# Kernel tuning notes

Hardware: AMD Instinct MI355X
Metric: run time of the kernel (lower is better)

Reference implementation:

```python
import jax, jax.numpy as jnp
import numpy as np

B, T, D, H, L, C = 64, 512, 256, 1024, 2, 128


def setup_inputs() -> dict:
    key = jax.random.key(0)
    ks = jax.random.split(key, 11)
    s = 0.05
    return {
        "x": jax.random.normal(ks[0], (B, T, D), dtype=jnp.float32),
        "W_ih0": jax.random.normal(ks[1], (4 * H, D), dtype=jnp.float32) * s,
        "W_hh0": jax.random.normal(ks[2], (4 * H, H), dtype=jnp.float32) * s,
        "b_ih0": jax.random.normal(ks[3], (4 * H,), dtype=jnp.float32) * s,
        "b_hh0": jax.random.normal(ks[4], (4 * H,), dtype=jnp.float32) * s,
        "W_ih1": jax.random.normal(ks[5], (4 * H, H), dtype=jnp.float32) * s,
        "W_hh1": jax.random.normal(ks[6], (4 * H, H), dtype=jnp.float32) * s,
        "b_ih1": jax.random.normal(ks[7], (4 * H,), dtype=jnp.float32) * s,
        "b_hh1": jax.random.normal(ks[8], (4 * H,), dtype=jnp.float32) * s,
        "W_fc": jax.random.normal(ks[9], (C, H), dtype=jnp.float32) * s,
        "b_fc": jax.random.normal(ks[10], (C,), dtype=jnp.float32) * s,
    }


def _lstm_cell(inp, h, c, Wi, Wh, bi, bh):
    # PyTorch LSTMCell: gates ordered i, f, g, o
    gates = inp @ Wi.T + bi + h @ Wh.T + bh  # [B, 4H]
    i, f, g, o = jnp.split(gates, 4, axis=-1)
    c_new = jax.nn.sigmoid(f) * c + jax.nn.sigmoid(i) * jnp.tanh(g)
    h_new = jax.nn.sigmoid(o) * jnp.tanh(c_new)
    return h_new, c_new


def reference(x, W_ih0, W_hh0, b_ih0, b_hh0, W_ih1, W_hh1, b_ih1, b_hh1, W_fc, b_fc):
    b = x.shape[0]
    h0 = jnp.zeros((b, H), x.dtype)
    init = (h0, h0, h0, h0)  # (h_l0, c_l0, h_l1, c_l1)

    def step(carry, x_t):
        h0_, c0_, h1_, c1_ = carry
        h0n, c0n = _lstm_cell(x_t, h0_, c0_, W_ih0, W_hh0, b_ih0, b_hh0)
        h1n, c1n = _lstm_cell(h0n, h1_, c1_, W_ih1, W_hh1, b_ih1, b_hh1)
        return (h0n, c0n, h1n, c1n), None

    xt = jnp.swapaxes(x, 0, 1)  # [T, B, D]
    (h0f, c0f, h1f, c1f), _ = jax.lax.scan(step, init, xt)
    return h1f @ W_fc.T + b_fc  # [B, num_classes]
```

## Files before the change

### kernel.cpp

```cpp
#include <hip/hip_runtime.h>
#include <hip/hip_bf16.h>

#define B_ 64
#define T_ 512
#define D_ 256
#define H_ 1024
#define RING 64
#define PS 260

typedef __attribute__((ext_vector_type(8))) short short8;
typedef __attribute__((ext_vector_type(4))) float floatx4;

__device__ __forceinline__ unsigned short f2bf(float f){
  unsigned u = __builtin_bit_cast(unsigned, f);
  u = (u + 0x7fffu + ((u >> 16) & 1u)) >> 16;
  return (unsigned short)u;
}

__device__ __forceinline__ short8 pack8(floatx4 a, floatx4 b){
  short8 r;
  r[0]=(short)f2bf(a[0]); r[1]=(short)f2bf(a[1]); r[2]=(short)f2bf(a[2]); r[3]=(short)f2bf(a[3]);
  r[4]=(short)f2bf(b[0]); r[5]=(short)f2bf(b[1]); r[6]=(short)f2bf(b[2]); r[7]=(short)f2bf(b[3]);
  return r;
}

__device__ __forceinline__ float sigm(float v){ return 1.f/(1.f+__expf(-v)); }
__device__ __forceinline__ float tanh_f(float v){ return 1.f - 2.f/(1.f+__expf(2.f*v)); }

__device__ __forceinline__ void gpoll(const unsigned long long* watch,
                                      unsigned& seen0, unsigned& seen1,
                                      unsigned tgt0, unsigned tgt1){
  if (__all(seen0 >= tgt0 && seen1 >= tgt1)) return;
  long g = 0;
  for (;;){
    unsigned long long v = __hip_atomic_load(watch, __ATOMIC_RELAXED, __HIP_MEMORY_SCOPE_AGENT);
    unsigned v0 = (unsigned)v, v1 = (unsigned)(v >> 32);
    seen0 = v0 > seen0 ? v0 : seen0;
    seen1 = v1 > seen1 ? v1 : seen1;
    if (__all(seen0 >= tgt0 && seen1 >= tgt1)) break;
    if (++g > (1L<<24)) break;
  }
}

__device__ __forceinline__ void lspin(unsigned* flag, unsigned tgt){
  long g = 0;
  while (__hip_atomic_load(flag, __ATOMIC_RELAXED, __HIP_MEMORY_SCOPE_WORKGROUP) < tgt){
    if (++g > (1L<<24)) break;
  }
}

template<int LAYER>
__device__ __forceinline__ void run_lstm(
    const float* __restrict__ x,
    const float* __restrict__ Wi, const float* __restrict__ Wh,
    const float* __restrict__ bi, const float* __restrict__ bh,
    unsigned* seq, unsigned short* h0h, unsigned short* h1h, float* h1f,
    int jbase, int j, int half,
    float* partial , float* c_st , float* biasv ,
    unsigned* rdy )
{
  constexpr int NK = LAYER ? 8 : 5;
  constexpr int KA = LAYER ? 1024 : 256;

  const int tid  = threadIdx.x;
  const int wave = tid >> 6;
  const int lane = tid & 63;
  const int n15  = lane & 15;
  const int kq   = (lane >> 4) * 8;

  short8 bfr[4][NK];
  #pragma unroll
  for (int nt = 0; nt < 4; nt++){
    int n   = nt*16 + n15;
    int row = (n >> 4)*H_ + jbase + (n & 15);
    #pragma unroll
    for (int ks = 0; ks < NK; ks++){
      int k = (LAYER ? (ks < 4 ? 1024 + wave*128 + ks*32 : wave*128 + (ks-4)*32)
                     : wave*160 + ks*32) + kq;
      const float* s = (k < KA) ? (Wi + (size_t)row*KA + k)
                                : (Wh + (size_t)row*H_ + (k - KA));
      bfr[nt][ks] = pack8(*(const floatx4*)s, *(const floatx4*)(s + 4));
    }
  }
  if (tid < 64){
    int col = (tid >> 4)*H_ + jbase + (tid & 15);
    biasv[tid] = bi[col] + bh[col];
  }
  c_st[tid & 511] = 0.f;
  if (tid == 0){ rdy[0] = 0u; rdy[1] = 0u; }
  __syncthreads();

  const unsigned long long* watch =
      (const unsigned long long*)seq + (size_t)(half*64 + lane);
  const bool isPoll = LAYER ? (wave == 0 || wave == 4) : (wave <= 1);

  unsigned seen0 = 0, seen1 = 0;
  unsigned long long vf = 0;

  for (int t = 0; t < T_; t++){
    { unsigned p0 = (unsigned)vf, p1 = (unsigned)(vf >> 32);
      seen0 = p0 > seen0 ? p0 : seen0;
      seen1 = p1 > seen1 ? p1 : seen1; }

    floatx4 acc[2][4];
    #pragma unroll
    for (int mt = 0; mt < 2; mt++)
      #pragma unroll
      for (int nt = 0; nt < 4; nt++)
        acc[mt][nt] = (floatx4)0.f;

    const unsigned short* h0t = h0h + ((size_t)((LAYER ? t : (t-1)) & (RING-1)) << 16);
    const unsigned short* h1t = h1h + ((size_t)((t-1) & (RING-1)) << 16);

    if constexpr (LAYER == 0){
      #pragma unroll
      for (int ks = 0; ks < NK; ks++){
        const int kb = wave*160 + ks*32;
        if (kb < D_){
          const int kk = kb + kq;
          short8 afr[2];
          #pragma unroll
          for (int mt = 0; mt < 2; mt++){
            const float* xs = x + ((size_t)(half*32 + mt*16 + n15)*T_ + t)*D_ + kk;
            afr[mt] = pack8(*(const floatx4*)xs, *(const floatx4*)(xs + 4));
          }
          #pragma unroll
          for (int mt = 0; mt < 2; mt++)
            #pragma unroll
            for (int nt = 0; nt < 4; nt++)
              acc[mt][nt] = __builtin_amdgcn_mfma_f32_16x16x32_bf16(afr[mt], bfr[nt][ks], acc[mt][nt], 0, 0, 0);
        }
      }
      __builtin_amdgcn_sched_barrier(0);
      if (wave == 0){
        gpoll(watch, seen0, seen1, 0u, (t >= RING) ? (unsigned)(t - RING + 1) : 0u);
      } else if (wave == 1){
        gpoll(watch, seen0, seen1, (unsigned)t, 0u);
        if (lane == 0) __hip_atomic_store(&rdy[0], (unsigned)(t + 1),
                                          __ATOMIC_RELAXED, __HIP_MEMORY_SCOPE_WORKGROUP);
      } else {
        lspin(&rdy[0], (unsigned)(t + 1));
      }
      __builtin_amdgcn_sched_barrier(0);
      if (t > 0){
        #pragma unroll
        for (int ks = 0; ks < NK; ks++){
          const int kb = wave*160 + ks*32;
          if (kb >= D_){
            const int hk = kb - D_ + kq;
            const unsigned short* p = h0t + ((hk >> 4) << 10) + (hk & 15);
            short8 afr[2];
            #pragma unroll
            for (int mt = 0; mt < 2; mt++)
              afr[mt] = *(const short8*)(p + ((half*32 + mt*16 + n15) << 4));
            #pragma unroll
            for (int mt = 0; mt < 2; mt++)
              #pragma unroll
              for (int nt = 0; nt < 4; nt++)
                acc[mt][nt] = __builtin_amdgcn_mfma_f32_16x16x32_bf16(afr[mt], bfr[nt][ks], acc[mt][nt], 0, 0, 0);
          }
        }
      }
    } else {
      if (wave == 4){
        gpoll(watch, seen0, seen1, 0u, (unsigned)t);
        if (lane == 0) __hip_atomic_store(&rdy[1], (unsigned)(t + 1),
                                          __ATOMIC_RELAXED, __HIP_MEMORY_SCOPE_WORKGROUP);
      } else {
        lspin(&rdy[1], (unsigned)(t + 1));
      }
      __builtin_amdgcn_sched_barrier(0);
      if (t > 0){
        #pragma unroll
        for (int ks = 0; ks < 4; ks++){
          const int hk = wave*128 + ks*32 + kq;
          const unsigned short* p = h1t + ((hk >> 4) << 10) + (hk & 15);
          short8 afr[2];
          #pragma unroll
          for (int mt = 0; mt < 2; mt++)
            afr[mt] = *(const short8*)(p + ((half*32 + mt*16 + n15) << 4));
          #pragma unroll
          for (int mt = 0; mt < 2; mt++)
            #pragma unroll
            for (int nt = 0; nt < 4; nt++)
              acc[mt][nt] = __builtin_amdgcn_mfma_f32_16x16x32_bf16(afr[mt], bfr[nt][ks], acc[mt][nt], 0, 0, 0);
        }
      }
      __builtin_amdgcn_sched_barrier(0);
      if (wave == 0){
        gpoll(watch, seen0, seen1, (unsigned)(t + 1), 0u);
        if (lane == 0) __hip_atomic_store(&rdy[0], (unsigned)(t + 1),
                                          __ATOMIC_RELAXED, __HIP_MEMORY_SCOPE_WORKGROUP);
      } else {
        lspin(&rdy[0], (unsigned)(t + 1));
      }
      __builtin_amdgcn_sched_barrier(0);
      #pragma unroll
      for (int ks = 4; ks < 8; ks++){
        const int hk = wave*128 + (ks-4)*32 + kq;
        const unsigned short* p = h0t + ((hk >> 4) << 10) + (hk & 15);
        short8 afr[2];
        #pragma unroll
        for (int mt = 0; mt < 2; mt++)
          afr[mt] = *(const short8*)(p + ((half*32 + mt*16 + n15) << 4));
        #pragma unroll
        for (int mt = 0; mt < 2; mt++)
          #pragma unroll
          for (int nt = 0; nt < 4; nt++)
            acc[mt][nt] = __builtin_amdgcn_mfma_f32_16x16x32_bf16(afr[mt], bfr[nt][ks], acc[mt][nt], 0, 0, 0);
      }
    }

    #pragma unroll
    for (int mt = 0; mt < 2; mt++)
      #pragma unroll
      for (int nt = 0; nt < 4; nt++){
        int n  = nt*16 + n15;
        int b0 = mt*16 + (lane >> 4)*4;
        *(floatx4*)(partial + (size_t)n*PS + wave*32 + b0) = acc[mt][nt];
      }
    __syncthreads();

    {
      int b = tid >> 4, jj = tid & 15;
      float g[4];
      #pragma unroll
      for (int q = 0; q < 4; q++){
        const float* p = partial + (size_t)(q*16 + jj)*PS + b;
        float s = biasv[q*16 + jj];
        #pragma unroll
        for (int ss = 0; ss < 8; ss++) s += p[ss*32];
        g[q] = s;
      }
      float co = c_st[tid];
      float si = sigm(g[0]), sf = sigm(g[1]), tg = tanh_f(g[2]), so = sigm(g[3]);
      float cn = sf*co + si*tg;
      float hn = so*tanh_f(cn);
      c_st[tid] = cn;
      unsigned hb = (unsigned)f2bf(hn);
      unsigned ob = (unsigned)__shfl_xor((int)hb, 1, 64);
      if (!(jj & 1)){
        unsigned pk = hb | (ob << 16);
        unsigned short* dst = (LAYER ? h1h : h0h)
                            + ((size_t)(t & (RING-1)) << 16)
                            + ((size_t)j << 10) + ((size_t)(half*32 + b) << 4) + jj;
        __hip_atomic_store((unsigned*)dst, pk, __ATOMIC_RELAXED, __HIP_MEMORY_SCOPE_AGENT);
      }
      if (LAYER == 1 && t == T_-1)
        h1f[(size_t)(half*32 + b)*H_ + jbase + jj] = hn;
    }
    if (isPoll)
      vf = __hip_atomic_load(watch, __ATOMIC_RELAXED, __HIP_MEMORY_SCOPE_AGENT);
    __syncthreads();
    if (tid == 0)
      __hip_atomic_store(seq + (size_t)(half*64 + j)*2 + LAYER, (unsigned)(t + 1),
                         __ATOMIC_RELAXED, __HIP_MEMORY_SCOPE_AGENT);
  }
}

__global__ __launch_bounds__(512, 2) void lstm_pk(
    const float* __restrict__ x,
    const float* __restrict__ Wih0, const float* __restrict__ Whh0,
    const float* __restrict__ bih0, const float* __restrict__ bhh0,
    const float* __restrict__ Wih1, const float* __restrict__ Whh1,
    const float* __restrict__ bih1, const float* __restrict__ bhh1,
    char* __restrict__ ws)
{
  __shared__ __align__(16) float partial[64*PS];
  __shared__ float c_st[512];
  __shared__ float biasv[64];
  __shared__ unsigned rdy[2];

  unsigned* seq       = (unsigned*)ws;
  unsigned short* h0h = (unsigned short*)(ws + (1<<20));
  unsigned short* h1h = (unsigned short*)(ws + (1<<20) + RING*B_*H_*2);
  float* h1f          = (float*)(ws + (1<<20) + 2*(size_t)RING*B_*H_*2);

  const int bid = blockIdx.x;
  if (bid < 128){
    run_lstm<0>(x, Wih0, Whh0, bih0, bhh0, seq, h0h, h1h, h1f,
                (bid & 63)*16, bid & 63, bid >> 6, partial, c_st, biasv, rdy);
  } else {
    const int r = bid - 128;
    run_lstm<1>(x, Wih1, Whh1, bih1, bhh1, seq, h0h, h1h, h1f,
                (r & 63)*16, r & 63, r >> 6, partial, c_st, biasv, rdy);
  }
}

__global__ __launch_bounds__(128) void fc_k(
    const float* __restrict__ h1f, const float* __restrict__ Wfc,
    const float* __restrict__ bfc, float* __restrict__ out)
{
  __shared__ float hv[1024];
  int b = blockIdx.x, c = threadIdx.x;
  for (int i = c; i < 1024; i += 128) hv[i] = h1f[(size_t)b*1024 + i];
  __syncthreads();
  const floatx4* w4 = (const floatx4*)(Wfc + (size_t)c*1024);
  const floatx4* h4 = (const floatx4*)hv;
  float acc = 0.f;
  #pragma unroll 8
  for (int k = 0; k < 256; k++){
    floatx4 wv = w4[k];
    floatx4 hh = h4[k];
    acc += wv[0]*hh[0] + wv[1]*hh[1] + wv[2]*hh[2] + wv[3]*hh[3];
  }
  out[(size_t)b*128 + c] = acc + bfc[c];
}

extern "C" void kernel_launch(void* const* d_in, const int* in_sizes, int n_in,
                              void* d_out, int out_size, void* d_ws, size_t ws_size,
                              hipStream_t stream)
{
  const float* x    = (const float*)d_in[0];
  const float* Wih0 = (const float*)d_in[1];
  const float* Whh0 = (const float*)d_in[2];
  const float* bih0 = (const float*)d_in[3];
  const float* bhh0 = (const float*)d_in[4];
  const float* Wih1 = (const float*)d_in[5];
  const float* Whh1 = (const float*)d_in[6];
  const float* bih1 = (const float*)d_in[7];
  const float* bhh1 = (const float*)d_in[8];
  const float* Wfc  = (const float*)d_in[9];
  const float* bfc  = (const float*)d_in[10];

  hipMemsetAsync(d_ws, 0, 4096, stream);

  lstm_pk<<<256, 512, 0, stream>>>(x, Wih0, Whh0, bih0, bhh0, Wih1, Whh1, bih1, bhh1, (char*)d_ws);

  const float* h1f = (const float*)((char*)d_ws + (1<<20) + 2*(size_t)RING*B_*H_*2);
  fc_k<<<64, 128, 0, stream>>>(h1f, Wfc, bfc, (float*)d_out);
}
```

Measured before the change: 3.507 ms.

## Split layer-1 K range per wave by source and raise MFMA wave priority

Layer 1 used to have every wave split its K slice between the recurrent h1 input and the h0 input. That forced two sequential poll and wait phases per step. Now each wave handles a contiguous 256-wide K slice: waves 0-3 cover the h0 input and waves 4-7 the h1 recurrent input. Each group waits only on its own ready flag, so h1 work can proceed without waiting for h0. s_setprio is also raised around the MFMA loops in both layers, so compute waves are favoured over polling waves, at the risk of delaying the pollers.

```diff
diff --git a/kernel.cpp b/kernel.cpp
--- a/kernel.cpp
+++ b/kernel.cpp
@@ -75,8 +75,7 @@
     int row = (n >> 4)*H_ + jbase + (n & 15);
     #pragma unroll
     for (int ks = 0; ks < NK; ks++){
-      int k = (LAYER ? (ks < 4 ? 1024 + wave*128 + ks*32 : wave*128 + (ks-4)*32)
-                     : wave*160 + ks*32) + kq;
+      int k = (LAYER ? wave*256 + ks*32 : wave*160 + ks*32) + kq;
       const float* s = (k < KA) ? (Wi + (size_t)row*KA + k)
                                 : (Wh + (size_t)row*H_ + (k - KA));
       bfr[nt][ks] = pack8(*(const floatx4*)s, *(const floatx4*)(s + 4));
@@ -113,6 +112,7 @@
     const unsigned short* h1t = h1h + ((size_t)((t-1) & (RING-1)) << 16);
 
     if constexpr (LAYER == 0){
+      __builtin_amdgcn_s_setprio(1);
       #pragma unroll
       for (int ks = 0; ks < NK; ks++){
         const int kb = wave*160 + ks*32;
@@ -131,6 +131,7 @@
               acc[mt][nt] = __builtin_amdgcn_mfma_f32_16x16x32_bf16(afr[mt], bfr[nt][ks], acc[mt][nt], 0, 0, 0);
         }
       }
+      __builtin_amdgcn_s_setprio(0);
       __builtin_amdgcn_sched_barrier(0);
       if (wave == 0){
         gpoll(watch, seen0, seen1, 0u, (t >= RING) ? (unsigned)(t - RING + 1) : 0u);
@@ -143,6 +144,7 @@
       }
       __builtin_amdgcn_sched_barrier(0);
       if (t > 0){
+        __builtin_amdgcn_s_setprio(1);
         #pragma unroll
         for (int ks = 0; ks < NK; ks++){
           const int kb = wave*160 + ks*32;
@@ -160,45 +162,32 @@
                 acc[mt][nt] = __builtin_amdgcn_mfma_f32_16x16x32_bf16(afr[mt], bfr[nt][ks], acc[mt][nt], 0, 0, 0);
           }
         }
+        __builtin_amdgcn_s_setprio(0);
       }
     } else {
-      if (wave == 4){
-        gpoll(watch, seen0, seen1, 0u, (unsigned)t);
-        if (lane == 0) __hip_atomic_store(&rdy[1], (unsigned)(t + 1),
-                                          __ATOMIC_RELAXED, __HIP_MEMORY_SCOPE_WORKGROUP);
-      } else {
-        lspin(&rdy[1], (unsigned)(t + 1));
-      }
-      __builtin_amdgcn_sched_barrier(0);
-      if (t > 0){
-        #pragma unroll
-        for (int ks = 0; ks < 4; ks++){
-          const int hk = wave*128 + ks*32 + kq;
-          const unsigned short* p = h1t + ((hk >> 4) << 10) + (hk & 15);
-          short8 afr[2];
-          #pragma unroll
-          for (int mt = 0; mt < 2; mt++)
-            afr[mt] = *(const short8*)(p + ((half*32 + mt*16 + n15) << 4));
-          #pragma unroll
-          for (int mt = 0; mt < 2; mt++)
-            #pragma unroll
-            for (int nt = 0; nt < 4; nt++)
-              acc[mt][nt] = __builtin_amdgcn_mfma_f32_16x16x32_bf16(afr[mt], bfr[nt][ks], acc[mt][nt], 0, 0, 0);
-        }
-      }
-      __builtin_amdgcn_sched_barrier(0);
       if (wave == 0){
         gpoll(watch, seen0, seen1, (unsigned)(t + 1), 0u);
         if (lane == 0) __hip_atomic_store(&rdy[0], (unsigned)(t + 1),
                                           __ATOMIC_RELAXED, __HIP_MEMORY_SCOPE_WORKGROUP);
+      } else if (wave == 4){
+        gpoll(watch, seen0, seen1, 0u, (unsigned)t);
+        if (lane == 0) __hip_atomic_store(&rdy[1], (unsigned)(t + 1),
+                                          __ATOMIC_RELAXED, __HIP_MEMORY_SCOPE_WORKGROUP);
+      } else if (wave < 4){
+        lspin(&rdy[0], (unsigned)(t + 1));
       } else {
-        lspin(&rdy[0], (unsigned)(t + 1));
+        lspin(&rdy[1], (unsigned)(t + 1));
       }
       __builtin_amdgcn_sched_barrier(0);
-      #pragma unroll
-      for (int ks = 4; ks < 8; ks++){
-        const int hk = wave*128 + (ks-4)*32 + kq;
-        const unsigned short* p = h0t + ((hk >> 4) << 10) + (hk & 15);
+      __builtin_amdgcn_s_setprio(1);
+      #pragma unroll
+      for (int ks = 0; ks < NK; ks++){
+        const int kb = wave*256 + ks*32;
+        if (kb >= KA && t == 0) continue;
+        const int kk = kb + kq;
+        const int hk = (kb < 1024) ? kk : (kk - 1024);
+        const unsigned short* sb = (kb < 1024) ? h0t : h1t;
+        const unsigned short* p = sb + ((hk >> 4) << 10) + (hk & 15);
         short8 afr[2];
         #pragma unroll
         for (int mt = 0; mt < 2; mt++)
@@ -209,6 +198,7 @@
           for (int nt = 0; nt < 4; nt++)
             acc[mt][nt] = __builtin_amdgcn_mfma_f32_16x16x32_bf16(afr[mt], bfr[nt][ks], acc[mt][nt], 0, 0, 0);
       }
+      __builtin_amdgcn_s_setprio(0);
     }
 
     #pragma unroll
```

After: 3.539 ms. About the same (+0.9%).
